# Kernel optimization log

Measured on AMD Instinct MI355X. Metric: run time of the kernel, lower is better.

## Reference

```python
import jax, jax.numpy as jnp
import numpy as np

B, S, H, D = 4, 2048, 8, 64


def init_offset(size, a=0.02, b=0.1, lo=8.0, hi=14.0):
    if size == 1:
        return jnp.array([(hi - lo) / 2], dtype=jnp.float32)
    x = jnp.log(jnp.expm1(jnp.linspace(a, b, size)))
    x = (x - x.min()) / (x.max() - x.min())
    return (x * abs(hi - lo) + lo).astype(jnp.float32)


def setup_inputs() -> dict:
    key = jax.random.key(0)
    k1, k2, k3 = jax.random.split(key, 3)
    qk = jax.random.normal(k1, (B, S, 2, H, D), dtype=jnp.float32)
    v = jax.random.normal(k2, (B, S, H, D), dtype=jnp.float32)
    n = jax.random.normal(k3, (B, S, H), dtype=jnp.float32)
    offset = init_offset(H)  # learned per-head offset parameter
    return {"qk": qk, "v": v, "n": n, "offset": offset}


def reference(qk, v, n, offset):
    # approx_fn = elu(x) + 1 (feature map), norm_fn = softplus, scale_B=True
    q = jax.nn.elu(qk[:, :, 0]) + 1.0  # (B,S,H,D)
    k = jax.nn.elu(qk[:, :, 1]) + 1.0  # (B,S,H,D)
    scale = 1.0 / jnp.sqrt(jnp.asarray(q.shape[-1], q.dtype))
    # outer product per position then causal prefix-sum over sequence
    kv = jnp.einsum('bshd,bsht->bshdt', k * scale, v)  # (B,S,H,D,D)
    kv = jnp.cumsum(kv, axis=1)
    out = jnp.einsum('bshd,bshdt->bsht', q, kv)  # (B,S,H,D)
    norm = jnp.exp(-jax.nn.softplus(n + offset))  # (B,S,H)
    return norm[:, :, :, None] * out
```

## Files before the change

### kernel.cpp

```cpp
#include <hip/hip_runtime.h>
#include <cstdint>

#define BB 4
#define SS 2048
#define HH 8
#define DD 64
#define CC 64
#define NCK (SS/CC)
#define BHH (BB*HH)

typedef __attribute__((ext_vector_type(8))) short  short8;
typedef __attribute__((ext_vector_type(4))) float  f32x4;
typedef __attribute__((ext_vector_type(4))) unsigned short us4;
typedef unsigned long long u64;

__device__ __forceinline__ float elu1(float x) {
    return x > 0.f ? x + 1.f : __expf(x);
}
__device__ __forceinline__ unsigned short f2bf(float f) {
    unsigned int u = __float_as_uint(f);
    u += 0x7FFFu + ((u >> 16) & 1u);
    return (unsigned short)(u >> 16);
}
__device__ __forceinline__ float bf2f(unsigned short h) {
    return __uint_as_float(((unsigned int)h) << 16);
}
#define SWZ(r,c) ((r) * DD + ((c) ^ (((r) & 7) << 3)))

template<int M0, int M1>
__device__ __forceinline__ void xpose4(float v[4], int lane) {
    {
        const bool hi = (lane & M0) != 0;
        float x0 = hi ? v[0] : v[1];
        float x1 = hi ? v[2] : v[3];
        float r0 = __shfl_xor(x0, M0);
        float r1 = __shfl_xor(x1, M0);
        if (hi) { v[0] = r0; v[2] = r1; } else { v[1] = r0; v[3] = r1; }
    }
    {
        const bool hi = (lane & M1) != 0;
        float x0 = hi ? v[0] : v[2];
        float x1 = hi ? v[1] : v[3];
        float r0 = __shfl_xor(x0, M1);
        float r1 = __shfl_xor(x1, M1);
        if (hi) { v[0] = r0; v[1] = r1; } else { v[2] = r0; v[3] = r1; }
    }
}

__device__ __forceinline__ u64 pack4bf(const float v[4]) {
    u64 r;
    r  = (u64)f2bf(v[0]);
    r |= (u64)f2bf(v[1]) << 16;
    r |= (u64)f2bf(v[2]) << 32;
    r |= (u64)f2bf(v[3]) << 48;
    return r;
}

__global__ __launch_bounds__(256) void state_kernel(
    const float* __restrict__ qk, const float* __restrict__ v,
    unsigned short* __restrict__ kws, unsigned short* __restrict__ vtws,
    u64* __restrict__ Sws)
{
    const int blk = blockIdx.x;
    const int bh = blk / NCK, c = blk % NCK;
    const int b = bh / HH, h = bh % HH;
    const int s0 = c * CC;

    __shared__ __align__(16) unsigned short kT[CC * DD];
    __shared__ __align__(16) unsigned short vT[CC * DD];

    const int tid = threadIdx.x, lane = tid & 63;

#pragma unroll
    for (int iter = 0; iter < 4; ++iter) {
        const int it = iter * 256 + tid;
        const int r = it >> 4, c0 = (it & 15) * 4;
        const int g = lane >> 4;
        const int rb = r - g;

        const size_t krow = (((size_t)(b * SS + s0 + r) * 2 + 1) * HH + h) * DD;

        float4 fk = *reinterpret_cast<const float4*>(qk + krow + c0);
        float kv4[4] = { elu1(fk.x) * 0.125f, elu1(fk.y) * 0.125f,
                         elu1(fk.z) * 0.125f, elu1(fk.w) * 0.125f };
        us4 uk; uk.x = f2bf(kv4[0]); uk.y = f2bf(kv4[1]);
                uk.z = f2bf(kv4[2]); uk.w = f2bf(kv4[3]);
        *reinterpret_cast<us4*>(kws + (size_t)blk * 4096 + SWZ(r, c0)) = uk;
        xpose4<16, 32>(kv4, lane);
        *reinterpret_cast<u64*>(&kT[SWZ(c0 + g, rb)]) = pack4bf(kv4);

        float4 fv = *reinterpret_cast<const float4*>(
            v + ((size_t)(b * SS + s0 + r) * HH + h) * DD + c0);
        float vv4[4] = { fv.x, fv.y, fv.z, fv.w };
        xpose4<16, 32>(vv4, lane);
        *reinterpret_cast<u64*>(&vT[SWZ(c0 + g, rb)]) = pack4bf(vv4);
    }
    __syncthreads();

#pragma unroll
    for (int j = 0; j < 2; ++j) {
        const int slot = j * 256 + tid;
        *reinterpret_cast<short8*>(vtws + (size_t)blk * 4096 + slot * 8) =
            *reinterpret_cast<const short8*>(&vT[slot * 8]);
    }

    const int lr = lane & 15, lk = (lane >> 4) * 8;
    const int wid = tid >> 6, mbase = wid * 16;
    f32x4 sc[4] = {};
#pragma unroll
    for (int kk = 0; kk < 2; ++kk) {
        short8 a = *reinterpret_cast<const short8*>(&vT[SWZ(mbase + lr, kk * 32 + lk)]);
#pragma unroll
        for (int nb = 0; nb < 4; ++nb) {
            short8 bk = *reinterpret_cast<const short8*>(&kT[SWZ(nb * 16 + lr, kk * 32 + lk)]);
            sc[nb] = __builtin_amdgcn_mfma_f32_16x16x32_bf16(a, bk, sc[nb], 0, 0, 0);
        }
    }
    const int crow = (lane >> 4) * 4;
#pragma unroll
    for (int nb = 0; nb < 4; ++nb) {
        float cv[4] = { sc[nb][0], sc[nb][1], sc[nb][2], sc[nb][3] };
        xpose4<1, 2>(cv, lane);
        const int t  = mbase + crow + (lane & 3);
        const int d0 = nb * 16 + (lr & ~3);
        Sws[(size_t)blk * 1024 + (SWZ(t, d0) >> 2)] = pack4bf(cv);
    }
}

__global__ __launch_bounds__(256, 4) void out_kernel(
    const float* __restrict__ qk, const float* __restrict__ nrm,
    const float* __restrict__ offset,
    const unsigned short* __restrict__ kws, const unsigned short* __restrict__ vtws,
    const u64* __restrict__ Sws, float* __restrict__ out)
{
    const int blk = blockIdx.x;
    const int bh = blk / NCK, c = blk % NCK;
    const int b = bh / HH, h = bh % HH;
    const int s0 = c * CC;

    __shared__ __align__(16) unsigned short qb[CC * DD];
    __shared__ __align__(16) unsigned short kb[CC * DD];
    __shared__ __align__(16) unsigned short vT[CC * DD];
    __shared__ __align__(16) unsigned short stk[CC * DD];

    const int tid = threadIdx.x, lane = tid & 63;
    const int wid = tid >> 6;

    {
        const unsigned short* gsrc[2] = { kws + (size_t)blk * 4096,
                                          vtws + (size_t)blk * 4096 };
        unsigned short* ldst[2] = { kb, vT };
#pragma unroll
        for (int bu = 0; bu < 2; ++bu) {
#pragma unroll
            for (int j = 0; j < 2; ++j) {
                const unsigned short* gp = gsrc[bu] + (size_t)(j * 256 + tid) * 8;
                __builtin_amdgcn_global_load_lds(
                    (const __attribute__((address_space(1))) void*)gp,
                    (__attribute__((address_space(3))) void*)(ldst[bu] + j * 2048 + wid * 512),
                    16, 0, 0);
            }
        }
    }

#pragma unroll
    for (int iter = 0; iter < 4; ++iter) {
        const int it = iter * 256 + tid;
        const int r = it >> 4, c0 = (it & 15) * 4;
        const size_t qrow = (((size_t)(b * SS + s0 + r) * 2 + 0) * HH + h) * DD;
        float4 fq = *reinterpret_cast<const float4*>(qk + qrow + c0);
        us4 uq; uq.x = f2bf(elu1(fq.x)); uq.y = f2bf(elu1(fq.y));
                uq.z = f2bf(elu1(fq.z)); uq.w = f2bf(elu1(fq.w));
        *reinterpret_cast<us4*>(&qb[SWZ(r, c0)]) = uq;
    }

    const int lr    = lane & 15;
    const int lk    = (lane >> 4) * 8;
    const int mbase = wid * 16;
    const int crow  = (lane >> 4) * 4;

    const float off = offset[h];
    float nv[4];
#pragma unroll
    for (int r = 0; r < 4; ++r) {
        const int s = s0 + mbase + crow + r;
        nv[r] = nrm[(size_t)(b * SS + s) * HH + h] + off;
    }

    float run[16] = {};
    {
        const u64* base = Sws + (size_t)bh * NCK * 1024 + (size_t)tid * 4;
        int j = 0;
        for (; j + 2 <= c; j += 2) {
            const u64* s0p = base + (size_t)j * 1024;
            const u64* s1p = s0p + 1024;
            u64 x0[4], x1[4];
#pragma unroll
            for (int w2 = 0; w2 < 4; ++w2) { x0[w2] = s0p[w2]; x1[w2] = s1p[w2]; }
#pragma unroll
            for (int w2 = 0; w2 < 4; ++w2) {
                run[w2 * 4 + 0] += bf2f((unsigned short)(x0[w2]))       + bf2f((unsigned short)(x1[w2]));
                run[w2 * 4 + 1] += bf2f((unsigned short)(x0[w2] >> 16)) + bf2f((unsigned short)(x1[w2] >> 16));
                run[w2 * 4 + 2] += bf2f((unsigned short)(x0[w2] >> 32)) + bf2f((unsigned short)(x1[w2] >> 32));
                run[w2 * 4 + 3] += bf2f((unsigned short)(x0[w2] >> 48)) + bf2f((unsigned short)(x1[w2] >> 48));
            }
        }
        if (j < c) {
            const u64* s0p = base + (size_t)j * 1024;
#pragma unroll
            for (int w2 = 0; w2 < 4; ++w2) {
                u64 x = s0p[w2];
                run[w2 * 4 + 0] += bf2f((unsigned short)(x));
                run[w2 * 4 + 1] += bf2f((unsigned short)(x >> 16));
                run[w2 * 4 + 2] += bf2f((unsigned short)(x >> 32));
                run[w2 * 4 + 3] += bf2f((unsigned short)(x >> 48));
            }
        }
    }
    u64* stk64 = reinterpret_cast<u64*>(stk);
#pragma unroll
    for (int w2 = 0; w2 < 4; ++w2) {
        float cv[4] = { run[w2 * 4 + 0], run[w2 * 4 + 1],
                        run[w2 * 4 + 2], run[w2 * 4 + 3] };
        stk64[(size_t)tid * 4 + w2] = pack4bf(cv);
    }

    __syncthreads();

    f32x4 acc[4] = {};
    f32x4 as4[4] = {};
#pragma unroll
    for (int kk = 0; kk < 2; ++kk) {
        short8 aq = *reinterpret_cast<const short8*>(&qb[SWZ(mbase + lr, kk * 32 + lk)]);
#pragma unroll
        for (int nb = 0; nb < 4; ++nb) {
            short8 bs = *reinterpret_cast<const short8*>(&stk[SWZ(nb * 16 + lr, kk * 32 + lk)]);
            acc[nb] = __builtin_amdgcn_mfma_f32_16x16x32_bf16(aq, bs, acc[nb], 0, 0, 0);
            short8 bk = *reinterpret_cast<const short8*>(&kb[SWZ(nb * 16 + lr, kk * 32 + lk)]);
            as4[nb] = __builtin_amdgcn_mfma_f32_16x16x32_bf16(aq, bk, as4[nb], 0, 0, 0);
        }
    }
    __syncthreads();

#pragma unroll
    for (int nb = 0; nb < 4; ++nb) {
#pragma unroll
        for (int r = 0; r < 4; ++r) {
            const int s_loc = mbase + crow + r;
            const int s2    = nb * 16 + lr;
            const float val = (s2 <= s_loc) ? as4[nb][r] : 0.f;
            kb[SWZ(s_loc, s2)] = f2bf(val);
        }
    }

#pragma unroll
    for (int kk = 0; kk < 2; ++kk) {
        short8 aa = *reinterpret_cast<const short8*>(&kb[SWZ(mbase + lr, kk * 32 + lk)]);
#pragma unroll
        for (int nb = 0; nb < 4; ++nb) {
            short8 bv = *reinterpret_cast<const short8*>(&vT[SWZ(nb * 16 + lr, kk * 32 + lk)]);
            acc[nb] = __builtin_amdgcn_mfma_f32_16x16x32_bf16(aa, bv, acc[nb], 0, 0, 0);
        }
    }

#pragma unroll
    for (int r = 0; r < 4; ++r) nv[r] = 1.f / (1.f + __expf(nv[r]));
#pragma unroll
    for (int nb = 0; nb < 4; ++nb) {
#pragma unroll
        for (int r = 0; r < 4; ++r) {
            const int s = s0 + mbase + crow + r;
            out[((size_t)(b * SS + s) * HH + h) * DD + nb * 16 + lr] = acc[nb][r] * nv[r];
        }
    }
}

extern "C" void kernel_launch(void* const* d_in, const int* in_sizes, int n_in,
                              void* d_out, int out_size, void* d_ws, size_t ws_size,
                              hipStream_t stream) {
    const float* qk     = (const float*)d_in[0];
    const float* v      = (const float*)d_in[1];
    const float* nrm    = (const float*)d_in[2];
    const float* offset = (const float*)d_in[3];
    float* out = (float*)d_out;

    const size_t TILE = (size_t)BHH * NCK * 4096;
    unsigned short* kws  = (unsigned short*)d_ws;
    unsigned short* vtws = kws + TILE;
    u64* Sws = (u64*)(vtws + TILE);

    state_kernel<<<dim3(BHH * NCK), dim3(256), 0, stream>>>(qk, v, kws, vtws, Sws);
    out_kernel<<<dim3(BHH * NCK), dim3(256), 0, stream>>>(qk, nrm, offset, kws, vtws, Sws, out);
}
```

Before: 118.2 us.

## Compute exclusive chunk-state prefix in last-arriving block; recompute K in out kernel

The state kernel now has each (batch, head) group count finished chunks with an atomic flag. The last block to arrive turns the per-chunk states into an exclusive prefix sum in place, so out_kernel loads its ready-made prefix state directly instead of summing up to 31 earlier chunk states. K is no longer written to workspace; out_kernel recomputes the scaled elu K from qk. This removes redundant prefix reads and the K round trip through memory, but makes one block per group do a serial 32-step scan and adds a memset launch.

Measured after the change: 288.4 us. 144% more time.

```diff
diff --git a/kernel.cpp b/kernel.cpp
--- a/kernel.cpp
+++ b/kernel.cpp
@@ -58,8 +58,8 @@
 
 __global__ __launch_bounds__(256) void state_kernel(
     const float* __restrict__ qk, const float* __restrict__ v,
-    unsigned short* __restrict__ kws, unsigned short* __restrict__ vtws,
-    u64* __restrict__ Sws)
+    unsigned short* __restrict__ vtws, u64* __restrict__ Sws,
+    int* __restrict__ flags)
 {
     const int blk = blockIdx.x;
     const int bh = blk / NCK, c = blk % NCK;
@@ -68,6 +68,7 @@
 
     __shared__ __align__(16) unsigned short kT[CC * DD];
     __shared__ __align__(16) unsigned short vT[CC * DD];
+    __shared__ int isLast;
 
     const int tid = threadIdx.x, lane = tid & 63;
 
@@ -79,13 +80,9 @@
         const int rb = r - g;
 
         const size_t krow = (((size_t)(b * SS + s0 + r) * 2 + 1) * HH + h) * DD;
-
         float4 fk = *reinterpret_cast<const float4*>(qk + krow + c0);
         float kv4[4] = { elu1(fk.x) * 0.125f, elu1(fk.y) * 0.125f,
                          elu1(fk.z) * 0.125f, elu1(fk.w) * 0.125f };
-        us4 uk; uk.x = f2bf(kv4[0]); uk.y = f2bf(kv4[1]);
-                uk.z = f2bf(kv4[2]); uk.w = f2bf(kv4[3]);
-        *reinterpret_cast<us4*>(kws + (size_t)blk * 4096 + SWZ(r, c0)) = uk;
         xpose4<16, 32>(kv4, lane);
         *reinterpret_cast<u64*>(&kT[SWZ(c0 + g, rb)]) = pack4bf(kv4);
 
@@ -125,13 +122,46 @@
         const int d0 = nb * 16 + (lr & ~3);
         Sws[(size_t)blk * 1024 + (SWZ(t, d0) >> 2)] = pack4bf(cv);
     }
+
+    __threadfence();
+    __syncthreads();
+    if (tid == 0) {
+        int old = __hip_atomic_fetch_add(&flags[bh], 1,
+                                         __ATOMIC_ACQ_REL, __HIP_MEMORY_SCOPE_AGENT);
+        isLast = (old == NCK - 1);
+    }
+    __syncthreads();
+    if (!isLast) return;
+    __threadfence();
+
+    u64* base = Sws + (size_t)bh * NCK * 1024 + (size_t)tid * 4;
+    float run[16] = {};
+    for (int j = 0; j < NCK; ++j) {
+        u64* p = base + (size_t)j * 1024;
+        u64 x[4];
+#pragma unroll
+        for (int w2 = 0; w2 < 4; ++w2) x[w2] = p[w2];
+#pragma unroll
+        for (int w2 = 0; w2 < 4; ++w2) {
+            float cv[4] = { run[w2 * 4 + 0], run[w2 * 4 + 1],
+                            run[w2 * 4 + 2], run[w2 * 4 + 3] };
+            p[w2] = pack4bf(cv);
+        }
+#pragma unroll
+        for (int w2 = 0; w2 < 4; ++w2) {
+            run[w2 * 4 + 0] += bf2f((unsigned short)(x[w2]));
+            run[w2 * 4 + 1] += bf2f((unsigned short)(x[w2] >> 16));
+            run[w2 * 4 + 2] += bf2f((unsigned short)(x[w2] >> 32));
+            run[w2 * 4 + 3] += bf2f((unsigned short)(x[w2] >> 48));
+        }
+    }
 }
 
 __global__ __launch_bounds__(256, 4) void out_kernel(
     const float* __restrict__ qk, const float* __restrict__ nrm,
     const float* __restrict__ offset,
-    const unsigned short* __restrict__ kws, const unsigned short* __restrict__ vtws,
-    const u64* __restrict__ Sws, float* __restrict__ out)
+    const unsigned short* __restrict__ vtws, const u64* __restrict__ Sws,
+    float* __restrict__ out)
 {
     const int blk = blockIdx.x;
     const int bh = blk / NCK, c = blk % NCK;
@@ -147,19 +177,20 @@
     const int wid = tid >> 6;
 
     {
-        const unsigned short* gsrc[2] = { kws + (size_t)blk * 4096,
-                                          vtws + (size_t)blk * 4096 };
-        unsigned short* ldst[2] = { kb, vT };
-#pragma unroll
-        for (int bu = 0; bu < 2; ++bu) {
-#pragma unroll
-            for (int j = 0; j < 2; ++j) {
-                const unsigned short* gp = gsrc[bu] + (size_t)(j * 256 + tid) * 8;
-                __builtin_amdgcn_global_load_lds(
-                    (const __attribute__((address_space(1))) void*)gp,
-                    (__attribute__((address_space(3))) void*)(ldst[bu] + j * 2048 + wid * 512),
-                    16, 0, 0);
-            }
+        const unsigned short* gS = (const unsigned short*)(Sws + (size_t)blk * 1024);
+        const unsigned short* gV = vtws + (size_t)blk * 4096;
+#pragma unroll
+        for (int j = 0; j < 2; ++j) {
+            const unsigned short* gp1 = gS + (size_t)(j * 256 + tid) * 8;
+            __builtin_amdgcn_global_load_lds(
+                (const __attribute__((address_space(1))) void*)gp1,
+                (__attribute__((address_space(3))) void*)(stk + j * 2048 + wid * 512),
+                16, 0, 0);
+            const unsigned short* gp2 = gV + (size_t)(j * 256 + tid) * 8;
+            __builtin_amdgcn_global_load_lds(
+                (const __attribute__((address_space(1))) void*)gp2,
+                (__attribute__((address_space(3))) void*)(vT + j * 2048 + wid * 512),
+                16, 0, 0);
         }
     }
 
@@ -168,10 +199,16 @@
         const int it = iter * 256 + tid;
         const int r = it >> 4, c0 = (it & 15) * 4;
         const size_t qrow = (((size_t)(b * SS + s0 + r) * 2 + 0) * HH + h) * DD;
+
         float4 fq = *reinterpret_cast<const float4*>(qk + qrow + c0);
         us4 uq; uq.x = f2bf(elu1(fq.x)); uq.y = f2bf(elu1(fq.y));
                 uq.z = f2bf(elu1(fq.z)); uq.w = f2bf(elu1(fq.w));
         *reinterpret_cast<us4*>(&qb[SWZ(r, c0)]) = uq;
+
+        float4 fk = *reinterpret_cast<const float4*>(qk + qrow + (size_t)HH * DD + c0);
+        us4 uk; uk.x = f2bf(elu1(fk.x) * 0.125f); uk.y = f2bf(elu1(fk.y) * 0.125f);
+                uk.z = f2bf(elu1(fk.z) * 0.125f); uk.w = f2bf(elu1(fk.w) * 0.125f);
+        *reinterpret_cast<us4*>(&kb[SWZ(r, c0)]) = uk;
     }
 
     const int lr    = lane & 15;
@@ -185,44 +222,6 @@
     for (int r = 0; r < 4; ++r) {
         const int s = s0 + mbase + crow + r;
         nv[r] = nrm[(size_t)(b * SS + s) * HH + h] + off;
-    }
-
-    float run[16] = {};
-    {
-        const u64* base = Sws + (size_t)bh * NCK * 1024 + (size_t)tid * 4;
-        int j = 0;
-        for (; j + 2 <= c; j += 2) {
-            const u64* s0p = base + (size_t)j * 1024;
-            const u64* s1p = s0p + 1024;
-            u64 x0[4], x1[4];
-#pragma unroll
-            for (int w2 = 0; w2 < 4; ++w2) { x0[w2] = s0p[w2]; x1[w2] = s1p[w2]; }
-#pragma unroll
-            for (int w2 = 0; w2 < 4; ++w2) {
-                run[w2 * 4 + 0] += bf2f((unsigned short)(x0[w2]))       + bf2f((unsigned short)(x1[w2]));
-                run[w2 * 4 + 1] += bf2f((unsigned short)(x0[w2] >> 16)) + bf2f((unsigned short)(x1[w2] >> 16));
-                run[w2 * 4 + 2] += bf2f((unsigned short)(x0[w2] >> 32)) + bf2f((unsigned short)(x1[w2] >> 32));
-                run[w2 * 4 + 3] += bf2f((unsigned short)(x0[w2] >> 48)) + bf2f((unsigned short)(x1[w2] >> 48));
-            }
-        }
-        if (j < c) {
-            const u64* s0p = base + (size_t)j * 1024;
-#pragma unroll
-            for (int w2 = 0; w2 < 4; ++w2) {
-                u64 x = s0p[w2];
-                run[w2 * 4 + 0] += bf2f((unsigned short)(x));
-                run[w2 * 4 + 1] += bf2f((unsigned short)(x >> 16));
-                run[w2 * 4 + 2] += bf2f((unsigned short)(x >> 32));
-                run[w2 * 4 + 3] += bf2f((unsigned short)(x >> 48));
-            }
-        }
-    }
-    u64* stk64 = reinterpret_cast<u64*>(stk);
-#pragma unroll
-    for (int w2 = 0; w2 < 4; ++w2) {
-        float cv[4] = { run[w2 * 4 + 0], run[w2 * 4 + 1],
-                        run[w2 * 4 + 2], run[w2 * 4 + 3] };
-        stk64[(size_t)tid * 4 + w2] = pack4bf(cv);
     }
 
     __syncthreads();
@@ -285,10 +284,11 @@
     float* out = (float*)d_out;
 
     const size_t TILE = (size_t)BHH * NCK * 4096;
-    unsigned short* kws  = (unsigned short*)d_ws;
-    unsigned short* vtws = kws + TILE;
+    unsigned short* vtws = (unsigned short*)d_ws;
     u64* Sws = (u64*)(vtws + TILE);
-
-    state_kernel<<<dim3(BHH * NCK), dim3(256), 0, stream>>>(qk, v, kws, vtws, Sws);
-    out_kernel<<<dim3(BHH * NCK), dim3(256), 0, stream>>>(qk, nrm, offset, kws, vtws, Sws, out);
-}
+    int* flags = (int*)(Sws + (size_t)BHH * NCK * 1024);
+
+    hipMemsetAsync(flags, 0, BHH * sizeof(int), stream);
+    state_kernel<<<dim3(BHH * NCK), dim3(256), 0, stream>>>(qk, v, vtws, Sws, flags);
+    out_kernel<<<dim3(BHH * NCK), dim3(256), 0, stream>>>(qk, nrm, offset, vtws, Sws, out);
+}
```
